# Optimization experiments

Measured on AMD Instinct MI355X. Metric: run time of the kernel, lower is better.

## Reference

```python
import jax, jax.numpy as jnp
import numpy as np

B, T, P, V, D, DINO, H, L = 32, 40, 256, 4096, 256, 384, 4, 2
HD = D // H          # head dim 64
DFF = 4 * D          # 1024
EPS = 1e-5


def setup_inputs() -> dict:
    key = jax.random.key(0)
    ks = iter(jax.random.split(key, 40))
    rn = lambda shape, s=0.02: jax.random.normal(next(ks), shape, jnp.float32) * s
    return dict(
        patches=jax.random.normal(next(ks), (B, P, DINO), jnp.float32),
        tokens=jax.random.randint(next(ks), (B, T), 0, V, jnp.int32),
        tok_emb=rn((V, D)),
        pos_emb=rn((1, T, D)),
        qkv_w=rn((L, 3 * D, D)), qkv_b=jnp.zeros((L, 3 * D), jnp.float32),
        out_w=rn((L, D, D)), out_b=jnp.zeros((L, D), jnp.float32),
        ln1_s=jnp.ones((L, D), jnp.float32), ln1_b=jnp.zeros((L, D), jnp.float32),
        w1=rn((L, DFF, D)), b1=jnp.zeros((L, DFF), jnp.float32),
        w2=rn((L, D, DFF)), b2=jnp.zeros((L, D), jnp.float32),
        ln2_s=jnp.ones((L, D), jnp.float32), ln2_b=jnp.zeros((L, D), jnp.float32),
        fus_w1=rn((D, DINO + D)), fus_b1=jnp.zeros((D,), jnp.float32),
        fus_w2=rn((D, D)), fus_b2=jnp.zeros((D,), jnp.float32),
        cls_w=rn((V, D)), cls_b=jnp.zeros((V,), jnp.float32),
    )


def _ln(x, s, b):
    m = jnp.mean(x, -1, keepdims=True)
    v = jnp.var(x, -1, keepdims=True)
    return (x - m) * jax.lax.rsqrt(v + EPS) * s + b


def _token_encoder(tokens, tok_emb, pos_emb, qkv_w, qkv_b, out_w, out_b,
                   ln1_s, ln1_b, w1, b1, w2, b2, ln2_s, ln2_b):
    # Causal full-sequence pass: output at position t equals re-running the
    # unmasked encoder on tokens[:, :t+1] and taking the last position.
    x = tok_emb[tokens] + pos_emb[:, :tokens.shape[1], :]   # [B,T,D]
    causal = jnp.triu(jnp.full((T, T), -1e9, jnp.float32), 1)  # [T,T]
    for l in range(L):  # fixed small layer count
        qkv = x @ qkv_w[l].T + qkv_b[l]                     # [B,T,3D]
        q, k, v = jnp.split(qkv, 3, axis=-1)
        q = q.reshape(B, T, H, HD).transpose(0, 2, 1, 3)    # [B,H,T,hd]
        k = k.reshape(B, T, H, HD).transpose(0, 2, 1, 3)
        v = v.reshape(B, T, H, HD).transpose(0, 2, 1, 3)
        scores = jnp.einsum('bhqd,bhkd->bhqk', q, k) / np.sqrt(HD).astype(np.float32)
        attn = jax.nn.softmax(scores + causal, axis=-1)
        ctx = jnp.einsum('bhqk,bhkd->bhqd', attn, v)        # [B,H,T,hd]
        ctx = ctx.transpose(0, 2, 1, 3).reshape(B, T, D)
        x = _ln(x + ctx @ out_w[l].T + out_b[l], ln1_s[l], ln1_b[l])
        h = jax.nn.relu(x @ w1[l].T + b1[l]) @ w2[l].T + b2[l]
        x = _ln(x + h, ln2_s[l], ln2_b[l])
    return x  # [B,T,D]


def reference(patches, tokens, tok_emb, pos_emb, qkv_w, qkv_b, out_w, out_b,
              ln1_s, ln1_b, w1, b1, w2, b2, ln2_s, ln2_b,
              fus_w1, fus_b1, fus_w2, fus_b2, cls_w, cls_b):
    enc = _token_encoder(tokens, tok_emb, pos_emb, qkv_w, qkv_b, out_w, out_b,
                         ln1_s, ln1_b, w1, b1, w2, b2, ln2_s, ln2_b)  # [B,T,D]
    # context for step 0 is zeros; step t>0 uses encoder output at position t-1
    ctx = jnp.concatenate([jnp.zeros((B, 1, D), enc.dtype), enc[:, :-1]], axis=1)  # [B,T,D]
    # fusion MLP: split the concat-linear into a patch part and a context part
    wp, wc = fus_w1[:, :DINO], fus_w1[:, DINO:]
    pproj = patches @ wp.T                                  # [B,P,D]
    cproj = ctx @ wc.T + fus_b1                             # [B,T,D]
    h = jax.nn.gelu(pproj[:, None, :, :] + cproj[:, :, None, :], approximate=False)  # [B,T,P,D]
    fused = h @ fus_w2.T + fus_b2                           # [B,T,P,D]
    # sigmoid+gather of the 4096-way logits == gather classifier rows, dot, sigmoid
    w_sel = cls_w[tokens]                                   # [B,T,D]
    b_sel = cls_b[tokens]                                   # [B,T]
    logits = jnp.einsum('btpd,btd->btp', fused, w_sel) + b_sel[:, :, None]
    probs = jax.nn.sigmoid(logits)                          # [B,T,P]
    return probs.transpose(0, 2, 1)                         # [B,P,T] == [B,256,40]
```

## Files before the change

kernel.cpp:

```cpp
#include <hip/hip_runtime.h>
#include <hip/hip_bf16.h>

#define B_ 32
#define T_ 40
#define P_ 256
#define V_ 4096
#define D_ 256
#define DINO_ 384
#define H_ 4
#define L_ 2
#define HD_ 64
#define DFF_ 1024
#define EPS_ 1e-5f

typedef __bf16 bf16;
typedef __bf16 bf16x8 __attribute__((ext_vector_type(8)));
typedef float f32x4 __attribute__((ext_vector_type(4)));

#define OFF_QKV 0
#define OFF_OUTW 393216
#define OFF_W1 524288
#define OFF_W2 1048576
#define OFF_FUS 1572864
#define WB_TOTAL 1736704
#define CONV_BLOCKS 848
#define PAT_BLOCKS 1536

__device__ __forceinline__ bf16x8 cvt8(const float* p) {
  float4 f0 = *(const float4*)p;
  float4 f1 = *(const float4*)(p + 4);
  bf16x8 v;
  v[0] = (bf16)f0.x; v[1] = (bf16)f0.y; v[2] = (bf16)f0.z; v[3] = (bf16)f0.w;
  v[4] = (bf16)f1.x; v[5] = (bf16)f1.y; v[6] = (bf16)f1.z; v[7] = (bf16)f1.w;
  return v;
}

__global__ __launch_bounds__(256) void prep_k(
    const int* __restrict__ tokens, const float* __restrict__ tok_emb,
    const float* __restrict__ pos_emb, float* __restrict__ x,
    const float* __restrict__ fus_w2, bf16* __restrict__ w2Tb,
    const float* __restrict__ qkv_w, const float* __restrict__ out_w,
    const float* __restrict__ w1, const float* __restrict__ w2,
    const float* __restrict__ fus_w1, bf16* __restrict__ wb,
    const float* __restrict__ patches, bf16* __restrict__ patb) {
  __shared__ float tile[32][33];
  int bi = blockIdx.x;
  int tid = threadIdx.x;
  if (bi < B_ * T_) {
    int t = bi % T_;
    x[bi * D_ + tid] = tok_emb[tokens[bi] * D_ + tid] + pos_emb[t * D_ + tid];
  } else if (bi < B_ * T_ + 64) {
    int tt = bi - B_ * T_;
    int bx = (tt & 7) * 32, by = (tt >> 3) * 32;
    int tx = tid & 31, ty = tid >> 5;
#pragma unroll
    for (int i = 0; i < 32; i += 8) tile[ty + i][tx] = fus_w2[(by + ty + i) * D_ + bx + tx];
    __syncthreads();
#pragma unroll
    for (int i = 0; i < 32; i += 8)
      w2Tb[(bx + ty + i) * D_ + by + tx] = (bf16)tile[tx][ty + i];
  } else if (bi < B_ * T_ + 64 + CONV_BLOCKS) {
    long f = (long)(bi - B_ * T_ - 64) * 2048 + tid * 8;
    const float* src;
    long off;
    if (f < OFF_OUTW)      { src = qkv_w;  off = f - OFF_QKV; }
    else if (f < OFF_W1)   { src = out_w;  off = f - OFF_OUTW; }
    else if (f < OFF_W2)   { src = w1;     off = f - OFF_W1; }
    else if (f < OFF_FUS)  { src = w2;     off = f - OFF_W2; }
    else                   { src = fus_w1; off = f - OFF_FUS; }
    *(bf16x8*)&wb[f] = cvt8(src + off);
  } else {
    long f = (long)(bi - B_ * T_ - 64 - CONV_BLOCKS) * 2048 + tid * 8;
    *(bf16x8*)&patb[f] = cvt8(patches + f);
  }
}

template <int ABF16, int OBF16, int RELU, int RESID>
__global__ __launch_bounds__(256) void gemm_k(
    const void* __restrict__ Av, const bf16* __restrict__ W,
    const float* __restrict__ bias, const float* __restrict__ resid,
    void* __restrict__ outv, int K, int lda, int ldw, int ldc) {
  __shared__ bf16 As[32 * 72];
  __shared__ bf16 Ws[32 * 72];
  const int tid = threadIdx.x;
  const int lane = tid & 63;
  const int wv = tid >> 6;
  const int mi = wv & 1, ni = wv >> 1;
  const int col = lane & 15, quad = lane >> 4;
  const int bn = blockIdx.x * 32, bm = blockIdx.y * 32;
  const int srow = tid >> 3, kc = (tid & 7) * 8;
  const float* Af = (const float*)Av;
  const bf16* Ab = (const bf16*)Av;
  const bf16* Wp = W + (long)(bn + srow) * ldw + kc;

  f32x4 acc = {0.f, 0.f, 0.f, 0.f};
  for (int kk = 0; kk < K; kk += 64) {
    if (ABF16)
      *(bf16x8*)&As[srow * 72 + kc] = *(const bf16x8*)(Ab + (long)(bm + srow) * lda + kk + kc);
    else
      *(bf16x8*)&As[srow * 72 + kc] = cvt8(Af + (long)(bm + srow) * lda + kk + kc);
    *(bf16x8*)&Ws[srow * 72 + kc] = *(const bf16x8*)(Wp + kk);
    __syncthreads();
#pragma unroll
    for (int ki = 0; ki < 2; ++ki) {
      bf16x8 afr = *(const bf16x8*)&As[(mi * 16 + col) * 72 + ki * 32 + quad * 8];
      bf16x8 bfr = *(const bf16x8*)&Ws[(ni * 16 + col) * 72 + ki * 32 + quad * 8];
      acc = __builtin_amdgcn_mfma_f32_16x16x32_bf16(afr, bfr, acc, 0, 0, 0);
    }
    __syncthreads();
  }
  const int n = bn + ni * 16 + col;
  float bv = bias ? bias[n] : 0.0f;
#pragma unroll
  for (int r = 0; r < 4; ++r) {
    int m = bm + mi * 16 + quad * 4 + r;
    float val = acc[r] + bv;
    if (RESID) val += resid[(long)m * D_ + n];
    if (RELU) val = fmaxf(val, 0.0f);
    if (OBF16) ((bf16*)outv)[(long)m * ldc + n] = (bf16)val;
    else ((float*)outv)[(long)m * ldc + n] = val;
  }
}

__global__ __launch_bounds__(256) void ln_k(const float* __restrict__ s,
                                            float* __restrict__ xout,
                                            const float* __restrict__ g,
                                            const float* __restrict__ be) {
  int wv = threadIdx.x >> 6, lane = threadIdx.x & 63;
  int m = blockIdx.x * 4 + wv;
  float4 v = *(const float4*)(s + (long)m * D_ + lane * 4);
  float sum = v.x + v.y + v.z + v.w;
  float ss = v.x * v.x + v.y * v.y + v.z * v.z + v.w * v.w;
#pragma unroll
  for (int mk = 1; mk < 64; mk <<= 1) {
    sum += __shfl_xor(sum, mk);
    ss += __shfl_xor(ss, mk);
  }
  float mean = sum * (1.0f / D_);
  float inv = rsqrtf(ss * (1.0f / D_) - mean * mean + EPS_);
  float4 g4 = *(const float4*)(g + lane * 4);
  float4 b4 = *(const float4*)(be + lane * 4);
  float4 o;
  o.x = (v.x - mean) * inv * g4.x + b4.x;
  o.y = (v.y - mean) * inv * g4.y + b4.y;
  o.z = (v.z - mean) * inv * g4.z + b4.z;
  o.w = (v.w - mean) * inv * g4.w + b4.w;
  *(float4*)(xout + (long)m * D_ + lane * 4) = o;
}

__global__ __launch_bounds__(256) void attn_k(const float* __restrict__ qkv,
                                              float* __restrict__ ctx) {
  __shared__ float q[20][HD_ + 1];
  __shared__ float k[T_][HD_ + 1];
  __shared__ float v[T_][HD_ + 1];
  __shared__ float s[20][T_ + 1];
  int h = blockIdx.x, b = blockIdx.y, zq = blockIdx.z;
  int r0 = zq * 20;
  int tid = threadIdx.x;
  for (int idx = tid; idx < T_ * HD_; idx += 256) {
    int t = idx >> 6, d = idx & 63;
    long base = (long)(b * T_ + t) * (3 * D_) + h * HD_ + d;
    k[t][d] = qkv[base + D_];
    v[t][d] = qkv[base + 2 * D_];
    if (t < 20) q[t][d] = qkv[(long)(b * T_ + r0 + t) * (3 * D_) + h * HD_ + d];
  }
  __syncthreads();
  for (int idx = tid; idx < 20 * T_; idx += 256) {
    int i = idx / T_, j = idx - i * T_;
    if (j <= r0 + i) {
      float acc = 0.f;
#pragma unroll
      for (int d = 0; d < HD_; ++d) acc += q[i][d] * k[j][d];
      s[i][j] = acc * 0.125f;
    }
  }
  __syncthreads();
  if (tid < 20) {
    int i = tid, hi = r0 + i;
    float mx = -1e30f;
    for (int j = 0; j <= hi; ++j) mx = fmaxf(mx, s[i][j]);
    float sum = 0.f;
    for (int j = 0; j <= hi; ++j) {
      float e = __expf(s[i][j] - mx);
      s[i][j] = e;
      sum += e;
    }
    float inv = 1.0f / sum;
    for (int j = 0; j <= hi; ++j) s[i][j] *= inv;
  }
  __syncthreads();
  for (int idx = tid; idx < 20 * HD_; idx += 256) {
    int i = idx >> 6, d = idx & 63;
    int hi = r0 + i;
    float acc = 0.f;
    for (int j = 0; j <= hi; ++j) acc += s[i][j] * v[j][d];
    ctx[(long)(b * T_ + hi) * D_ + h * HD_ + d] = acc;
  }
}

__global__ __launch_bounds__(256) void fuse3_k(
    const bf16* __restrict__ patb, const float* __restrict__ xbuf,
    const float* __restrict__ cls_w, const bf16* __restrict__ fusb,
    const bf16* __restrict__ w2Tb, const float* __restrict__ fus_b1,
    const int* __restrict__ tokens, float* __restrict__ pprojT,
    float* __restrict__ cw) {
  __shared__ bf16 As[32 * 72];
  __shared__ bf16 Ws[32 * 72];
  const int tid = threadIdx.x;
  const int lane = tid & 63;
  const int wv = tid >> 6;
  const int mi = wv & 1, ni = wv >> 1;
  const int col = lane & 15, quad = lane >> 4;
  const int bn = blockIdx.x * 32;
  const int y = blockIdx.y;
  const int srow = tid >> 3, kc = (tid & 7) * 8;

  int job, bm;
  if (y < 256) { job = 0; bm = y * 32; }
  else if (y < 296) { job = 1; bm = (y - 256) * 32; }
  else { job = 2; bm = (y - 296) * 32; }
  const int gm = bm + srow;

  const bf16* Wp;
  int K = D_;
  bool zeroA = false;
  const float* Apf = nullptr;
  const bf16* Apb = nullptr;
  if (job == 0) {
    Apb = patb + (long)gm * DINO_;
    Wp = fusb + (long)(bn + srow) * 640 + kc;
    K = DINO_;
  } else if (job == 1) {
    int t = gm % T_;
    zeroA = (t == 0);
    Apf = xbuf + (long)(zeroA ? gm : gm - 1) * D_;
    Wp = fusb + 384 + (long)(bn + srow) * 640 + kc;
  } else {
    Apf = cls_w + (long)tokens[gm] * D_;
    Wp = w2Tb + (long)(bn + srow) * D_ + kc;
  }

  f32x4 acc = {0.f, 0.f, 0.f, 0.f};
  bf16x8 z8 = {};
  for (int kk = 0; kk < K; kk += 64) {
    bf16x8 av;
    if (job == 0) av = *(const bf16x8*)(Apb + kk + kc);
    else if (zeroA) av = z8;
    else av = cvt8(Apf + kk + kc);
    *(bf16x8*)&As[srow * 72 + kc] = av;
    *(bf16x8*)&Ws[srow * 72 + kc] = *(const bf16x8*)(Wp + kk);
    __syncthreads();
#pragma unroll
    for (int ki = 0; ki < 2; ++ki) {
      bf16x8 afr = *(const bf16x8*)&As[(mi * 16 + col) * 72 + ki * 32 + quad * 8];
      bf16x8 bfr = *(const bf16x8*)&Ws[(ni * 16 + col) * 72 + ki * 32 + quad * 8];
      acc = __builtin_amdgcn_mfma_f32_16x16x32_bf16(afr, bfr, acc, 0, 0, 0);
    }
    __syncthreads();
  }
  const int n = bn + ni * 16 + col;
  if (job == 0) {
#pragma unroll
    for (int r4 = 0; r4 < 4; ++r4) {
      int m = bm + mi * 16 + quad * 4 + r4;
      int b = m >> 8, p = m & 255;
      pprojT[(long)b * (D_ * P_) + (long)n * P_ + p] = acc[r4];
    }
  } else if (job == 1) {
    float bv = fus_b1[n];
#pragma unroll
    for (int r4 = 0; r4 < 4; ++r4) {
      int m = bm + mi * 16 + quad * 4 + r4;
      cw[(long)m * (2 * D_) + n * 2] = acc[r4] + bv;
    }
  } else {
#pragma unroll
    for (int r4 = 0; r4 < 4; ++r4) {
      int m = bm + mi * 16 + quad * 4 + r4;
      cw[(long)m * (2 * D_) + n * 2 + 1] = acc[r4];
    }
  }
}

__global__ __launch_bounds__(256) void final_k(const float* __restrict__ pprojT,
                                               const float* __restrict__ cw,
                                               const int* __restrict__ tokens,
                                               const float* __restrict__ cls_w,
                                               const float* __restrict__ cls_b,
                                               const float* __restrict__ fus_b2,
                                               float* __restrict__ out) {
  __shared__ float2 cws[4][D_];
  int tid = threadIdx.x;
  int lane = tid & 63, wv = tid >> 6;
  int p = blockIdx.x * 64 + lane;
  int t = blockIdx.y * 4 + wv;
  int b = blockIdx.z;
  int mbase = b * T_ + blockIdx.y * 4;
  for (int idx = tid; idx < 4 * D_; idx += 256) {
    int tt = idx >> 8, e = idx & 255;
    cws[tt][e] = ((const float2*)cw)[(long)(mbase + tt) * D_ + e];
  }
  __syncthreads();

  int m = b * T_ + t;
  int tok = tokens[m];
  const float* cr = cls_w + (long)tok * D_;
  float bacc = 0.f;
#pragma unroll
  for (int i = 0; i < 4; ++i) bacc += cr[lane + i * 64] * fus_b2[lane + i * 64];
#pragma unroll
  for (int mk = 1; mk < 64; mk <<= 1) bacc += __shfl_xor(bacc, mk);
  float beff = bacc + cls_b[tok];

  const float* ppb = pprojT + (long)b * (D_ * P_);
  float acc = 0.f;
#pragma unroll 8
  for (int e = 0; e < D_; ++e) {
    float pp = ppb[e * P_ + p];
    float2 c = cws[wv][e];
    float x = pp + c.x;
    float x2 = x * x;
    float u = x * fmaf(-0.1029432f, x2, -2.3022083f);
    float ex = __builtin_amdgcn_exp2f(u);
    float r = __builtin_amdgcn_rcpf(1.0f + ex);
    acc = fmaf(x * r, c.y, acc);
  }
  float logit = acc + beff;
  float es = __builtin_amdgcn_exp2f(-1.4426950408889634f * logit);
  out[(long)(b * P_ + p) * T_ + t] = __builtin_amdgcn_rcpf(1.0f + es);
}

extern "C" void kernel_launch(void* const* d_in, const int* in_sizes, int n_in, void* d_out,
                              int out_size, void* d_ws, size_t ws_size, hipStream_t stream) {
  const float* patches = (const float*)d_in[0];
  const int* tokens = (const int*)d_in[1];
  const float* tok_emb = (const float*)d_in[2];
  const float* pos_emb = (const float*)d_in[3];
  const float* qkv_w = (const float*)d_in[4];
  const float* qkv_b = (const float*)d_in[5];
  const float* out_w = (const float*)d_in[6];
  const float* out_b = (const float*)d_in[7];
  const float* ln1_s = (const float*)d_in[8];
  const float* ln1_b = (const float*)d_in[9];
  const float* w1 = (const float*)d_in[10];
  const float* b1 = (const float*)d_in[11];
  const float* w2 = (const float*)d_in[12];
  const float* b2 = (const float*)d_in[13];
  const float* ln2_s = (const float*)d_in[14];
  const float* ln2_b = (const float*)d_in[15];
  const float* fus_w1 = (const float*)d_in[16];
  const float* fus_b1 = (const float*)d_in[17];
  const float* fus_w2 = (const float*)d_in[18];
  const float* fus_b2 = (const float*)d_in[19];
  const float* cls_w = (const float*)d_in[20];
  const float* cls_b = (const float*)d_in[21];
  float* out = (float*)d_out;

  const int MT = B_ * T_;
  float* x = (float*)d_ws;
  float* qkvbuf = x + MT * D_;
  float* attbuf = qkvbuf + MT * 3 * D_;
  float* s = attbuf + MT * D_;
  float* pprojT = s + MT * D_;
  float* cwbuf = pprojT + (long)B_ * D_ * P_;
  bf16* wb = (bf16*)(cwbuf + MT * D_ * 2);
  bf16* w2Tb = wb + WB_TOTAL;
  bf16* patb = w2Tb + D_ * D_;
  bf16* hb = patb + (long)B_ * P_ * DINO_;

  prep_k<<<MT + 64 + CONV_BLOCKS + PAT_BLOCKS, 256, 0, stream>>>(
      tokens, tok_emb, pos_emb, x, fus_w2, w2Tb, qkv_w, out_w, w1, w2, fus_w1, wb,
      patches, patb);

  for (int l = 0; l < L_; ++l) {
    gemm_k<0, 0, 0, 0><<<dim3(24, 40), 256, 0, stream>>>(
        x, wb + OFF_QKV + (long)l * 3 * D_ * D_, qkv_b + l * 3 * D_, nullptr, qkvbuf,
        D_, D_, D_, 3 * D_);
    attn_k<<<dim3(H_, B_, 2), 256, 0, stream>>>(qkvbuf, attbuf);
    gemm_k<0, 0, 0, 1><<<dim3(8, 40), 256, 0, stream>>>(
        attbuf, wb + OFF_OUTW + (long)l * D_ * D_, out_b + l * D_, x, s, D_, D_, D_, D_);
    ln_k<<<MT / 4, 256, 0, stream>>>(s, x, ln1_s + l * D_, ln1_b + l * D_);
    gemm_k<0, 1, 1, 0><<<dim3(32, 40), 256, 0, stream>>>(
        x, wb + OFF_W1 + (long)l * DFF_ * D_, b1 + l * DFF_, nullptr, hb, D_, D_, D_, DFF_);
    gemm_k<1, 0, 0, 1><<<dim3(8, 40), 256, 0, stream>>>(
        hb, wb + OFF_W2 + (long)l * D_ * DFF_, b2 + l * D_, x, s, DFF_, DFF_, DFF_, D_);
    ln_k<<<MT / 4, 256, 0, stream>>>(s, x, ln2_s + l * D_, ln2_b + l * D_);
  }

  fuse3_k<<<dim3(8, 336), 256, 0, stream>>>(patb, x, cls_w, wb + OFF_FUS, w2Tb,
                                            fus_b1, tokens, pprojT, cwbuf);

  final_k<<<dim3(4, 10, 32), 256, 0, stream>>>(pprojT, cwbuf, tokens, cls_w, cls_b,
                                               fus_b2, out);
}
```

Baseline: 257.5 us.

## Fuse residual and LayerNorm into GEMM epilogue and enlarge GEMM tiles to 64x64

The out-projection and FFN2 GEMMs now compute a full 32x256 row block per workgroup. They add bias and residual, then apply LayerNorm in the epilogue using a cross-wave reduction in shared memory. This removes the separate ln_k launches and the intermediate s buffer. The QKV, FFN1 and fusion GEMMs move from 32x32 to 64x64 tiles, with each wave computing four MFMA tiles for more operand reuse. The trade-off is that the fused LN GEMMs launch only 40 workgroups, which leaves most compute units idle during those stages.

```diff
diff --git a/kernel.cpp b/kernel.cpp
--- a/kernel.cpp
+++ b/kernel.cpp
@@ -75,77 +75,180 @@
   }
 }
 
-template <int ABF16, int OBF16, int RELU, int RESID>
-__global__ __launch_bounds__(256) void gemm_k(
+template <int ABF16, int OBF16, int RELU>
+__global__ __launch_bounds__(256) void gemm64_k(
     const void* __restrict__ Av, const bf16* __restrict__ W,
-    const float* __restrict__ bias, const float* __restrict__ resid,
-    void* __restrict__ outv, int K, int lda, int ldw, int ldc) {
-  __shared__ bf16 As[32 * 72];
-  __shared__ bf16 Ws[32 * 72];
+    const float* __restrict__ bias, void* __restrict__ outv,
+    int K, int lda, int ldw, int ldc) {
+  __shared__ bf16 As[64 * 72];
+  __shared__ bf16 Ws[64 * 72];
   const int tid = threadIdx.x;
   const int lane = tid & 63;
   const int wv = tid >> 6;
-  const int mi = wv & 1, ni = wv >> 1;
   const int col = lane & 15, quad = lane >> 4;
-  const int bn = blockIdx.x * 32, bm = blockIdx.y * 32;
+  const int bn = blockIdx.x * 64, bm = blockIdx.y * 64;
+  const float* Af = (const float*)Av;
+  const bf16* Ab = (const bf16*)Av;
+
+  f32x4 acc[4];
+#pragma unroll
+  for (int i = 0; i < 4; ++i) acc[i] = (f32x4){0.f, 0.f, 0.f, 0.f};
+
+  for (int kk = 0; kk < K; kk += 64) {
+#pragma unroll
+    for (int it = 0; it < 2; ++it) {
+      int c = tid + it * 256;
+      int row = c >> 3, kc = (c & 7) * 8;
+      if (ABF16)
+        *(bf16x8*)&As[row * 72 + kc] = *(const bf16x8*)(Ab + (long)(bm + row) * lda + kk + kc);
+      else
+        *(bf16x8*)&As[row * 72 + kc] = cvt8(Af + (long)(bm + row) * lda + kk + kc);
+      *(bf16x8*)&Ws[row * 72 + kc] = *(const bf16x8*)(W + (long)(bn + row) * ldw + kk + kc);
+    }
+    __syncthreads();
+#pragma unroll
+    for (int ki = 0; ki < 2; ++ki) {
+      bf16x8 bfr = *(const bf16x8*)&Ws[(wv * 16 + col) * 72 + ki * 32 + quad * 8];
+#pragma unroll
+      for (int i = 0; i < 4; ++i) {
+        bf16x8 afr = *(const bf16x8*)&As[(i * 16 + col) * 72 + ki * 32 + quad * 8];
+        acc[i] = __builtin_amdgcn_mfma_f32_16x16x32_bf16(afr, bfr, acc[i], 0, 0, 0);
+      }
+    }
+    __syncthreads();
+  }
+  const int n = bn + wv * 16 + col;
+  float bv = bias ? bias[n] : 0.0f;
+#pragma unroll
+  for (int i = 0; i < 4; ++i) {
+#pragma unroll
+    for (int r = 0; r < 4; ++r) {
+      int m = bm + i * 16 + quad * 4 + r;
+      float val = acc[i][r] + bv;
+      if (RELU) val = fmaxf(val, 0.0f);
+      if (OBF16) ((bf16*)outv)[(long)m * ldc + n] = (bf16)val;
+      else ((float*)outv)[(long)m * ldc + n] = val;
+    }
+  }
+}
+
+template <int ABF16>
+__global__ __launch_bounds__(256) void gemmln_k(
+    const void* __restrict__ Av, const bf16* __restrict__ W,
+    const float* __restrict__ bias, const float* __restrict__ resid,
+    const float* __restrict__ lng, const float* __restrict__ lnb,
+    float* __restrict__ xout, int K) {
+  __shared__ bf16 As[32 * 72];
+  __shared__ bf16 Ws[256 * 72];
+  __shared__ float2 wred[4][32];
+  const int tid = threadIdx.x;
+  const int lane = tid & 63;
+  const int wv = tid >> 6;
+  const int col = lane & 15, quad = lane >> 4;
+  const int bm = blockIdx.x * 32;
   const int srow = tid >> 3, kc = (tid & 7) * 8;
   const float* Af = (const float*)Av;
   const bf16* Ab = (const bf16*)Av;
-  const bf16* Wp = W + (long)(bn + srow) * ldw + kc;
-
-  f32x4 acc = {0.f, 0.f, 0.f, 0.f};
+
+  f32x4 acc[2][4];
+#pragma unroll
+  for (int mt = 0; mt < 2; ++mt)
+#pragma unroll
+    for (int nt = 0; nt < 4; ++nt) acc[mt][nt] = (f32x4){0.f, 0.f, 0.f, 0.f};
+
   for (int kk = 0; kk < K; kk += 64) {
     if (ABF16)
-      *(bf16x8*)&As[srow * 72 + kc] = *(const bf16x8*)(Ab + (long)(bm + srow) * lda + kk + kc);
+      *(bf16x8*)&As[srow * 72 + kc] = *(const bf16x8*)(Ab + (long)(bm + srow) * K + kk + kc);
     else
-      *(bf16x8*)&As[srow * 72 + kc] = cvt8(Af + (long)(bm + srow) * lda + kk + kc);
-    *(bf16x8*)&Ws[srow * 72 + kc] = *(const bf16x8*)(Wp + kk);
+      *(bf16x8*)&As[srow * 72 + kc] = cvt8(Af + (long)(bm + srow) * K + kk + kc);
+#pragma unroll
+    for (int i = 0; i < 8; ++i) {
+      int c = tid + i * 256;
+      int r = c >> 3, k2 = (c & 7) * 8;
+      *(bf16x8*)&Ws[r * 72 + k2] = *(const bf16x8*)(W + (long)r * K + kk + k2);
+    }
     __syncthreads();
 #pragma unroll
     for (int ki = 0; ki < 2; ++ki) {
-      bf16x8 afr = *(const bf16x8*)&As[(mi * 16 + col) * 72 + ki * 32 + quad * 8];
-      bf16x8 bfr = *(const bf16x8*)&Ws[(ni * 16 + col) * 72 + ki * 32 + quad * 8];
-      acc = __builtin_amdgcn_mfma_f32_16x16x32_bf16(afr, bfr, acc, 0, 0, 0);
-    }
-    __syncthreads();
-  }
-  const int n = bn + ni * 16 + col;
-  float bv = bias ? bias[n] : 0.0f;
-#pragma unroll
-  for (int r = 0; r < 4; ++r) {
-    int m = bm + mi * 16 + quad * 4 + r;
-    float val = acc[r] + bv;
-    if (RESID) val += resid[(long)m * D_ + n];
-    if (RELU) val = fmaxf(val, 0.0f);
-    if (OBF16) ((bf16*)outv)[(long)m * ldc + n] = (bf16)val;
-    else ((float*)outv)[(long)m * ldc + n] = val;
-  }
-}
-
-__global__ __launch_bounds__(256) void ln_k(const float* __restrict__ s,
-                                            float* __restrict__ xout,
-                                            const float* __restrict__ g,
-                                            const float* __restrict__ be) {
-  int wv = threadIdx.x >> 6, lane = threadIdx.x & 63;
-  int m = blockIdx.x * 4 + wv;
-  float4 v = *(const float4*)(s + (long)m * D_ + lane * 4);
-  float sum = v.x + v.y + v.z + v.w;
-  float ss = v.x * v.x + v.y * v.y + v.z * v.z + v.w * v.w;
-#pragma unroll
-  for (int mk = 1; mk < 64; mk <<= 1) {
-    sum += __shfl_xor(sum, mk);
-    ss += __shfl_xor(ss, mk);
-  }
-  float mean = sum * (1.0f / D_);
-  float inv = rsqrtf(ss * (1.0f / D_) - mean * mean + EPS_);
-  float4 g4 = *(const float4*)(g + lane * 4);
-  float4 b4 = *(const float4*)(be + lane * 4);
-  float4 o;
-  o.x = (v.x - mean) * inv * g4.x + b4.x;
-  o.y = (v.y - mean) * inv * g4.y + b4.y;
-  o.z = (v.z - mean) * inv * g4.z + b4.z;
-  o.w = (v.w - mean) * inv * g4.w + b4.w;
-  *(float4*)(xout + (long)m * D_ + lane * 4) = o;
+#pragma unroll
+      for (int nt = 0; nt < 4; ++nt) {
+        bf16x8 bfr = *(const bf16x8*)&Ws[(wv * 64 + nt * 16 + col) * 72 + ki * 32 + quad * 8];
+#pragma unroll
+        for (int mt = 0; mt < 2; ++mt) {
+          bf16x8 afr = *(const bf16x8*)&As[(mt * 16 + col) * 72 + ki * 32 + quad * 8];
+          acc[mt][nt] = __builtin_amdgcn_mfma_f32_16x16x32_bf16(afr, bfr, acc[mt][nt], 0, 0, 0);
+        }
+      }
+    }
+    __syncthreads();
+  }
+
+  float biasv[4], gv[4], bvv[4];
+#pragma unroll
+  for (int nt = 0; nt < 4; ++nt) {
+    int n = wv * 64 + nt * 16 + col;
+    biasv[nt] = bias[n];
+    gv[nt] = lng[n];
+    bvv[nt] = lnb[n];
+  }
+  float rsum[2][4], rss[2][4];
+#pragma unroll
+  for (int mt = 0; mt < 2; ++mt)
+#pragma unroll
+    for (int r = 0; r < 4; ++r) {
+      int m = bm + mt * 16 + quad * 4 + r;
+      float s = 0.f, q = 0.f;
+#pragma unroll
+      for (int nt = 0; nt < 4; ++nt) {
+        int n = wv * 64 + nt * 16 + col;
+        float v = acc[mt][nt][r] + biasv[nt] + resid[(long)m * D_ + n];
+        acc[mt][nt][r] = v;
+        s += v;
+        q += v * v;
+      }
+      rsum[mt][r] = s;
+      rss[mt][r] = q;
+    }
+#pragma unroll
+  for (int mk = 1; mk < 16; mk <<= 1)
+#pragma unroll
+    for (int mt = 0; mt < 2; ++mt)
+#pragma unroll
+      for (int r = 0; r < 4; ++r) {
+        rsum[mt][r] += __shfl_xor(rsum[mt][r], mk);
+        rss[mt][r] += __shfl_xor(rss[mt][r], mk);
+      }
+  if (col == 0) {
+#pragma unroll
+    for (int mt = 0; mt < 2; ++mt)
+#pragma unroll
+      for (int r = 0; r < 4; ++r) {
+        float2 p; p.x = rsum[mt][r]; p.y = rss[mt][r];
+        wred[wv][mt * 16 + quad * 4 + r] = p;
+      }
+  }
+  __syncthreads();
+#pragma unroll
+  for (int mt = 0; mt < 2; ++mt)
+#pragma unroll
+    for (int r = 0; r < 4; ++r) {
+      int ml = mt * 16 + quad * 4 + r;
+      float s = 0.f, q = 0.f;
+#pragma unroll
+      for (int w = 0; w < 4; ++w) {
+        float2 p = wred[w][ml];
+        s += p.x;
+        q += p.y;
+      }
+      float mean = s * (1.0f / D_);
+      float inv = rsqrtf(q * (1.0f / D_) - mean * mean + EPS_);
+#pragma unroll
+      for (int nt = 0; nt < 4; ++nt) {
+        int n = wv * 64 + nt * 16 + col;
+        xout[(long)(bm + ml) * D_ + n] =
+            (acc[mt][nt][r] - mean) * inv * gv[nt] + bvv[nt];
+      }
+    }
 }
 
 __global__ __launch_bounds__(256) void attn_k(const float* __restrict__ qkv,
@@ -204,81 +307,86 @@
     const bf16* __restrict__ w2Tb, const float* __restrict__ fus_b1,
     const int* __restrict__ tokens, float* __restrict__ pprojT,
     float* __restrict__ cw) {
-  __shared__ bf16 As[32 * 72];
-  __shared__ bf16 Ws[32 * 72];
+  __shared__ bf16 As[64 * 72];
+  __shared__ bf16 Ws[64 * 72];
   const int tid = threadIdx.x;
   const int lane = tid & 63;
   const int wv = tid >> 6;
-  const int mi = wv & 1, ni = wv >> 1;
   const int col = lane & 15, quad = lane >> 4;
-  const int bn = blockIdx.x * 32;
+  const int bn = blockIdx.x * 64;
   const int y = blockIdx.y;
-  const int srow = tid >> 3, kc = (tid & 7) * 8;
-
   int job, bm;
-  if (y < 256) { job = 0; bm = y * 32; }
-  else if (y < 296) { job = 1; bm = (y - 256) * 32; }
-  else { job = 2; bm = (y - 296) * 32; }
-  const int gm = bm + srow;
-
-  const bf16* Wp;
-  int K = D_;
-  bool zeroA = false;
-  const float* Apf = nullptr;
-  const bf16* Apb = nullptr;
+  if (y < 128) { job = 0; bm = y * 64; }
+  else if (y < 148) { job = 1; bm = (y - 128) * 64; }
+  else { job = 2; bm = (y - 148) * 64; }
+  const int K = (job == 0) ? DINO_ : D_;
+
+  f32x4 acc[4];
+#pragma unroll
+  for (int i = 0; i < 4; ++i) acc[i] = (f32x4){0.f, 0.f, 0.f, 0.f};
+  bf16x8 z8 = {};
+
+  for (int kk = 0; kk < K; kk += 64) {
+#pragma unroll
+    for (int it = 0; it < 2; ++it) {
+      int c = tid + it * 256;
+      int row = c >> 3, kc = (c & 7) * 8;
+      int gm = bm + row;
+      bf16x8 av;
+      const bf16* wp;
+      if (job == 0) {
+        av = *(const bf16x8*)(patb + (long)gm * DINO_ + kk + kc);
+        wp = fusb + (long)(bn + row) * 640 + kk + kc;
+      } else if (job == 1) {
+        int t = gm % T_;
+        av = (t == 0) ? z8 : cvt8(xbuf + (long)(gm - 1) * D_ + kk + kc);
+        wp = fusb + 384 + (long)(bn + row) * 640 + kk + kc;
+      } else {
+        av = cvt8(cls_w + (long)tokens[gm] * D_ + kk + kc);
+        wp = w2Tb + (long)(bn + row) * D_ + kk + kc;
+      }
+      *(bf16x8*)&As[row * 72 + kc] = av;
+      *(bf16x8*)&Ws[row * 72 + kc] = *(const bf16x8*)wp;
+    }
+    __syncthreads();
+#pragma unroll
+    for (int ki = 0; ki < 2; ++ki) {
+      bf16x8 bfr = *(const bf16x8*)&Ws[(wv * 16 + col) * 72 + ki * 32 + quad * 8];
+#pragma unroll
+      for (int i = 0; i < 4; ++i) {
+        bf16x8 afr = *(const bf16x8*)&As[(i * 16 + col) * 72 + ki * 32 + quad * 8];
+        acc[i] = __builtin_amdgcn_mfma_f32_16x16x32_bf16(afr, bfr, acc[i], 0, 0, 0);
+      }
+    }
+    __syncthreads();
+  }
+  const int n = bn + wv * 16 + col;
   if (job == 0) {
-    Apb = patb + (long)gm * DINO_;
-    Wp = fusb + (long)(bn + srow) * 640 + kc;
-    K = DINO_;
-  } else if (job == 1) {
-    int t = gm % T_;
-    zeroA = (t == 0);
-    Apf = xbuf + (long)(zeroA ? gm : gm - 1) * D_;
-    Wp = fusb + 384 + (long)(bn + srow) * 640 + kc;
-  } else {
-    Apf = cls_w + (long)tokens[gm] * D_;
-    Wp = w2Tb + (long)(bn + srow) * D_ + kc;
-  }
-
-  f32x4 acc = {0.f, 0.f, 0.f, 0.f};
-  bf16x8 z8 = {};
-  for (int kk = 0; kk < K; kk += 64) {
-    bf16x8 av;
-    if (job == 0) av = *(const bf16x8*)(Apb + kk + kc);
-    else if (zeroA) av = z8;
-    else av = cvt8(Apf + kk + kc);
-    *(bf16x8*)&As[srow * 72 + kc] = av;
-    *(bf16x8*)&Ws[srow * 72 + kc] = *(const bf16x8*)(Wp + kk);
-    __syncthreads();
-#pragma unroll
-    for (int ki = 0; ki < 2; ++ki) {
-      bf16x8 afr = *(const bf16x8*)&As[(mi * 16 + col) * 72 + ki * 32 + quad * 8];
-      bf16x8 bfr = *(const bf16x8*)&Ws[(ni * 16 + col) * 72 + ki * 32 + quad * 8];
-      acc = __builtin_amdgcn_mfma_f32_16x16x32_bf16(afr, bfr, acc, 0, 0, 0);
-    }
-    __syncthreads();
-  }
-  const int n = bn + ni * 16 + col;
-  if (job == 0) {
-#pragma unroll
-    for (int r4 = 0; r4 < 4; ++r4) {
-      int m = bm + mi * 16 + quad * 4 + r4;
-      int b = m >> 8, p = m & 255;
-      pprojT[(long)b * (D_ * P_) + (long)n * P_ + p] = acc[r4];
-    }
+#pragma unroll
+    for (int i = 0; i < 4; ++i)
+#pragma unroll
+      for (int r = 0; r < 4; ++r) {
+        int m = bm + i * 16 + quad * 4 + r;
+        int b = m >> 8, p = m & 255;
+        pprojT[(long)b * (D_ * P_) + (long)n * P_ + p] = acc[i][r];
+      }
   } else if (job == 1) {
     float bv = fus_b1[n];
 #pragma unroll
-    for (int r4 = 0; r4 < 4; ++r4) {
-      int m = bm + mi * 16 + quad * 4 + r4;
-      cw[(long)m * (2 * D_) + n * 2] = acc[r4] + bv;
-    }
+    for (int i = 0; i < 4; ++i)
+#pragma unroll
+      for (int r = 0; r < 4; ++r) {
+        int m = bm + i * 16 + quad * 4 + r;
+        cw[(long)m * (2 * D_) + n * 2] = acc[i][r] + bv;
+      }
   } else {
 #pragma unroll
-    for (int r4 = 0; r4 < 4; ++r4) {
-      int m = bm + mi * 16 + quad * 4 + r4;
-      cw[(long)m * (2 * D_) + n * 2 + 1] = acc[r4];
-    }
+    for (int i = 0; i < 4; ++i)
+#pragma unroll
+      for (int r = 0; r < 4; ++r) {
+        int m = bm + i * 16 + quad * 4 + r;
+        cw[(long)m * (2 * D_) + n * 2 + 1] = acc[i][r];
+      }
   }
 }
 
@@ -360,8 +468,7 @@
   float* x = (float*)d_ws;
   float* qkvbuf = x + MT * D_;
   float* attbuf = qkvbuf + MT * 3 * D_;
-  float* s = attbuf + MT * D_;
-  float* pprojT = s + MT * D_;
+  float* pprojT = attbuf + MT * D_;
   float* cwbuf = pprojT + (long)B_ * D_ * P_;
   bf16* wb = (bf16*)(cwbuf + MT * D_ * 2);
   bf16* w2Tb = wb + WB_TOTAL;
@@ -373,21 +480,21 @@
       patches, patb);
 
   for (int l = 0; l < L_; ++l) {
-    gemm_k<0, 0, 0, 0><<<dim3(24, 40), 256, 0, stream>>>(
-        x, wb + OFF_QKV + (long)l * 3 * D_ * D_, qkv_b + l * 3 * D_, nullptr, qkvbuf,
+    gemm64_k<0, 0, 0><<<dim3(12, 20), 256, 0, stream>>>(
+        x, wb + OFF_QKV + (long)l * 3 * D_ * D_, qkv_b + l * 3 * D_, qkvbuf,
         D_, D_, D_, 3 * D_);
     attn_k<<<dim3(H_, B_, 2), 256, 0, stream>>>(qkvbuf, attbuf);
-    gemm_k<0, 0, 0, 1><<<dim3(8, 40), 256, 0, stream>>>(
-        attbuf, wb + OFF_OUTW + (long)l * D_ * D_, out_b + l * D_, x, s, D_, D_, D_, D_);
-    ln_k<<<MT / 4, 256, 0, stream>>>(s, x, ln1_s + l * D_, ln1_b + l * D_);
-    gemm_k<0, 1, 1, 0><<<dim3(32, 40), 256, 0, stream>>>(
-        x, wb + OFF_W1 + (long)l * DFF_ * D_, b1 + l * DFF_, nullptr, hb, D_, D_, D_, DFF_);
-    gemm_k<1, 0, 0, 1><<<dim3(8, 40), 256, 0, stream>>>(
-        hb, wb + OFF_W2 + (long)l * D_ * DFF_, b2 + l * D_, x, s, DFF_, DFF_, DFF_, D_);
-    ln_k<<<MT / 4, 256, 0, stream>>>(s, x, ln2_s + l * D_, ln2_b + l * D_);
-  }
-
-  fuse3_k<<<dim3(8, 336), 256, 0, stream>>>(patb, x, cls_w, wb + OFF_FUS, w2Tb,
+    gemmln_k<0><<<40, 256, 0, stream>>>(
+        attbuf, wb + OFF_OUTW + (long)l * D_ * D_, out_b + l * D_, x,
+        ln1_s + l * D_, ln1_b + l * D_, x, D_);
+    gemm64_k<0, 1, 1><<<dim3(16, 20), 256, 0, stream>>>(
+        x, wb + OFF_W1 + (long)l * DFF_ * D_, b1 + l * DFF_, hb, D_, D_, D_, DFF_);
+    gemmln_k<1><<<40, 256, 0, stream>>>(
+        hb, wb + OFF_W2 + (long)l * D_ * DFF_, b2 + l * D_, x,
+        ln2_s + l * D_, ln2_b + l * D_, x, DFF_);
+  }
+
+  fuse3_k<<<dim3(4, 168), 256, 0, stream>>>(patb, x, cls_w, wb + OFF_FUS, w2Tb,
                                             fus_b1, tokens, pprojT, cwbuf);
 
   final_k<<<dim3(4, 10, 32), 256, 0, stream>>>(pprojT, cwbuf, tokens, cls_w, cls_b,
```

Result: slower. 284.9 us (+10.6%).
